# Kernel tuning notes

Hardware: AMD Instinct MI355X
Metric: run time of the kernel (lower is better)

Reference implementation:

```python
import jax, jax.numpy as jnp
import numpy as np

# ---- config (mirrors cfg in the torch module) ----
L_CIOU, L_CONF, L_CLS, L_ATTN = 2.0, 1.0, 1.0, 5.0
H_IN, W_IN, STRIDE, NUM_CLS = 1024, 1024, 4, 2
SIGMA = 1.5  # gaussian sigma for attention target
FOCAL_ALPHA, FOCAL_GAMMA = 0.25, 2.0
EPS = 1e-7


def setup_inputs() -> dict:
    key = jax.random.key(0)
    ks = jax.random.split(key, 6)
    B = 16
    fh, fw = H_IN // STRIDE, W_IN // STRIDE
    HW = fh * fw
    raw_grid = jax.random.normal(ks[0], (B, HW, 5 + NUM_CLS), dtype=jnp.float32)
    sal = jax.random.normal(ks[1], (B, 32, fh, fw), dtype=jnp.float32)
    N = 256
    bi = jax.random.randint(ks[2], (N,), 0, B).astype(jnp.float32)
    cxcy = jax.random.uniform(ks[3], (N, 2), minval=0.05, maxval=0.95)
    wh = jax.random.uniform(ks[4], (N, 2), minval=0.02, maxval=0.15)
    cls = jax.random.randint(ks[5], (N,), 0, NUM_CLS).astype(jnp.float32)
    targets = jnp.concatenate([bi[:, None], cxcy, wh, cls[:, None]], axis=1)
    return {"raw_grid": raw_grid, "sal": sal, "targets": targets}


def _ciou(p, t):
    """Complete IoU loss; p, t: (..., 4) cxcywh. Returns (...,)."""
    px1, py1 = p[..., 0] - p[..., 2] / 2, p[..., 1] - p[..., 3] / 2
    px2, py2 = p[..., 0] + p[..., 2] / 2, p[..., 1] + p[..., 3] / 2
    tx1, ty1 = t[..., 0] - t[..., 2] / 2, t[..., 1] - t[..., 3] / 2
    tx2, ty2 = t[..., 0] + t[..., 2] / 2, t[..., 1] + t[..., 3] / 2
    inter = (jnp.clip(jnp.minimum(px2, tx2) - jnp.maximum(px1, tx1), 0, None) *
             jnp.clip(jnp.minimum(py2, ty2) - jnp.maximum(py1, ty1), 0, None))
    union = p[..., 2] * p[..., 3] + t[..., 2] * t[..., 3] - inter
    iou = inter / (union + EPS)
    c2 = ((jnp.maximum(px2, tx2) - jnp.minimum(px1, tx1)) ** 2 +
          (jnp.maximum(py2, ty2) - jnp.minimum(py1, ty1)) ** 2 + EPS)
    d2 = (p[..., 0] - t[..., 0]) ** 2 + (p[..., 1] - t[..., 1]) ** 2
    v = (4.0 / (jnp.pi ** 2)) * (jnp.arctan(t[..., 2] / (t[..., 3] + EPS)) -
                                 jnp.arctan(p[..., 2] / (p[..., 3] + EPS))) ** 2
    alpha = jax.lax.stop_gradient(v / (1 - iou + v + EPS))
    return 1 - iou + d2 / c2 + alpha * v


def _decode_boxes(raw, fh, fw):
    """raw: (B, HW, 5+C) -> decoded boxes (B, HW, 4) and conf prob (B, HW)."""
    gy, gx = jnp.meshgrid(jnp.arange(fh, dtype=jnp.float32),
                          jnp.arange(fw, dtype=jnp.float32), indexing='ij')
    gx, gy = gx.reshape(-1), gy.reshape(-1)  # (HW,)
    cx = (jax.nn.sigmoid(raw[..., 0]) + gx) / fw
    cy = (jax.nn.sigmoid(raw[..., 1]) + gy) / fh
    w = jnp.exp(jnp.clip(raw[..., 2], -4, 4)) / fw
    h = jnp.exp(jnp.clip(raw[..., 3], -4, 4)) / fh
    conf = jax.nn.sigmoid(raw[..., 4])
    return jnp.stack([cx, cy, w, h], axis=-1), conf


def _assign(targets, B, fh, fw):
    """Vectorized FCOS-style assignment (replaces the per-target python loop).
    Each target emits 10 candidate writes: 3x3 neighborhood (conditioned on the
    cell centre lying inside the GT box) plus the unconditional centre cell.
    Last-write-wins semantics of the torch loop are reproduced with a
    scatter-max over a unique write priority."""
    N = targets.shape[0]
    HW = fh * fw
    bi = targets[:, 0].astype(jnp.int32)
    cx, cy, w, h = targets[:, 1], targets[:, 2], targets[:, 3], targets[:, 4]
    cls = targets[:, 5].astype(jnp.int32)
    gi = (cx * fw).astype(jnp.int32)
    gj = (cy * fh).astype(jnp.int32)
    dx = jnp.array([-1, -1, -1, 0, 0, 0, 1, 1, 1], jnp.int32)  # torch loop order
    dy = jnp.array([-1, 0, 1, -1, 0, 1, -1, 0, 1], jnp.int32)
    nx, ny = gi[:, None] + dx, gj[:, None] + dy               # (N, 9)
    inb = (nx >= 0) & (nx < fw) & (ny >= 0) & (ny < fh)
    ccx = (nx.astype(jnp.float32) + 0.5) / fw
    ccy = (ny.astype(jnp.float32) + 0.5) / fh
    inside = ((jnp.abs(ccx - cx[:, None]) <= w[:, None] / 2) &
              (jnp.abs(ccy - cy[:, None]) <= h[:, None] / 2))
    v9 = inb & inside
    c9 = ny * fw + nx
    cc = (jnp.minimum(gj, fh - 1) * fw + jnp.minimum(gi, fw - 1))[:, None]
    cells = jnp.concatenate([c9, cc], axis=1)                  # (N, 10)
    valid = jnp.concatenate([v9, jnp.ones((N, 1), bool)], axis=1)
    prio = (jnp.arange(N, dtype=jnp.int32)[:, None] * 10 +
            jnp.arange(10, dtype=jnp.int32)[None, :])          # unique per write
    PAD = B * HW
    flat = jnp.where(valid, bi[:, None] * HW + cells, PAD).reshape(-1)
    prio = jnp.where(valid, prio, -1).reshape(-1)
    win = jnp.full(PAD + 1, -1, jnp.int32).at[flat].max(prio)
    is_win = (prio >= 0) & (prio == win[flat])
    flat_w = jnp.where(is_win, flat, PAD)  # losers/invalid -> padding slot
    boxes = jnp.broadcast_to(targets[:, None, 1:5], (N, 10, 4)).reshape(-1, 4)
    tgt_box = jnp.zeros((PAD + 1, 4), jnp.float32).at[flat_w].set(boxes)[:PAD]
    clsb = jnp.broadcast_to(cls[:, None], (N, 10)).reshape(-1)
    tgt_cls = jnp.zeros(PAD + 1, jnp.int32).at[flat_w].set(clsb)[:PAD]
    obj = (win[:PAD] >= 0).astype(jnp.float32)
    return obj.reshape(B, HW), tgt_box.reshape(B, HW, 4), tgt_cls.reshape(B, HW)


def _attn_loss(sal, targets):
    """Batched Gaussian build + scatter-max (replaces per-target host loop)."""
    B, C, H, W = sal.shape
    gy, gx = jnp.meshgrid(jnp.arange(H, dtype=jnp.float32),
                          jnp.arange(W, dtype=jnp.float32), indexing='ij')
    bi = targets[:, 0].astype(jnp.int32)
    tx = targets[:, 1] * W
    ty = targets[:, 2] * H
    d2 = ((gx[None] - tx[:, None, None]) ** 2 +
          (gy[None] - ty[:, None, None]) ** 2)                 # (N, H, W)
    g = jnp.exp(-d2 / (2.0 * SIGMA ** 2))
    mask = jnp.zeros((B, H, W), jnp.float32).at[bi].max(g)     # scatter-max
    sal_mean = sal.mean(axis=1)                                # (B, H, W)
    return jnp.mean((sal_mean - mask) ** 2)


def reference(raw_grid, sal, targets):
    B, HW, _ = raw_grid.shape
    fh, fw = H_IN // STRIDE, W_IN // STRIDE
    loss_attn = _attn_loss(sal, targets)  # single saliency map (len==1 mean)

    pred_box, conf = _decode_boxes(raw_grid, fh, fw)
    obj, tgt_box, tgt_cls = _assign(targets, B, fh, fw)

    num_pos = jnp.sum(obj)
    norm = jnp.maximum(num_pos, 1.0)

    # focal BCE on confidence (all cells); stable via logits
    z = raw_grid[..., 4]
    bce = obj * jax.nn.softplus(-z) + (1 - obj) * jax.nn.softplus(z)
    pt = jnp.where(obj > 0, conf, 1 - conf)
    a_t = jnp.where(obj > 0, FOCAL_ALPHA, 1 - FOCAL_ALPHA)
    loss_conf = jnp.sum(a_t * (1 - pt) ** FOCAL_GAMMA * bce) / norm

    # CIoU over positive cells only (masked mean)
    loss_ciou = jnp.sum(_ciou(pred_box, tgt_box) * obj) / norm

    # cross-entropy over positive cells only
    logp = jax.nn.log_softmax(raw_grid[..., 5:], axis=-1)
    nll = -jnp.take_along_axis(logp, tgt_cls[..., None], axis=-1)[..., 0]
    loss_cls = jnp.sum(nll * obj) / norm

    return (L_CIOU * loss_ciou + L_CONF * loss_conf +
            L_CLS * loss_cls + L_ATTN * loss_attn)
```

## Files before the change

kernel.cpp:

```cpp
#include <hip/hip_runtime.h>
#include <math.h>

#define FH 256
#define FW 256
#define HW (FH * FW)
#define BATCH 16
#define NTGT 256
#define NCH 32
#define EPS_ 1e-7f

__device__ __forceinline__ float sigmoidf_(float x) {
    return 1.0f / (1.0f + expf(-x));
}
__device__ __forceinline__ float softplusf_(float x) {
    return fmaxf(x, 0.0f) + log1pf(expf(-fabsf(x)));
}

__global__ __launch_bounds__(256) void init_kernel(float* __restrict__ mask,
                                                   int* __restrict__ win) {
    int i = blockIdx.x * 256 + threadIdx.x;
    if (i < BATCH * HW) {
        mask[i] = 0.0f;
        win[i] = -1;
    }
}

__global__ __launch_bounds__(256) void scatter_kernel(const float* __restrict__ targets,
                                                      float* __restrict__ mask,
                                                      int* __restrict__ win) {
    int n = blockIdx.x;
    float bif = targets[n * 6 + 0];
    float cx  = targets[n * 6 + 1];
    float cy  = targets[n * 6 + 2];
    float w   = targets[n * 6 + 3];
    float h   = targets[n * 6 + 4];
    int bi = (int)bif;

    if (threadIdx.x == 0) {
        int gi = (int)(cx * (float)FW);
        int gj = (int)(cy * (float)FH);
#pragma unroll
        for (int k = 0; k < 9; ++k) {
            int dxv = k / 3 - 1;
            int dyv = k % 3 - 1;
            int nx = gi + dxv, ny = gj + dyv;
            bool inb = (nx >= 0) && (nx < FW) && (ny >= 0) && (ny < FH);
            float ccx = ((float)nx + 0.5f) / (float)FW;
            float ccy = ((float)ny + 0.5f) / (float)FH;
            bool inside = (fabsf(ccx - cx) <= w * 0.5f) && (fabsf(ccy - cy) <= h * 0.5f);
            if (inb && inside) {
                atomicMax(&win[bi * HW + ny * FW + nx], n * 10 + k);
            }
        }
        int cell = min(gj, FH - 1) * FW + min(gi, FW - 1);
        atomicMax(&win[bi * HW + cell], n * 10 + 9);
    }

    float tx = cx * (float)FW;
    float ty = cy * (float)FH;
    int itx = (int)tx, ity = (int)ty;
    int x0 = max(0, itx - 12), x1 = min(FW - 1, itx + 12);
    int y0 = max(0, ity - 12), y1 = min(FH - 1, ity + 12);
    int nxw = x1 - x0 + 1;
    int tot = nxw * (y1 - y0 + 1);
    unsigned int* mrow = (unsigned int*)(mask + bi * HW);
    for (int i = threadIdx.x; i < tot; i += blockDim.x) {
        int xx = x0 + i % nxw;
        int yy = y0 + i / nxw;
        float ddx = (float)xx - tx;
        float ddy = (float)yy - ty;
        float g = expf(-(ddx * ddx + ddy * ddy) / 4.5f);
        atomicMax(&mrow[yy * FW + xx], __float_as_uint(g));
    }
}

__global__ __launch_bounds__(256) void main_kernel(const float* __restrict__ raw,
                                                   const float* __restrict__ sal,
                                                   const float* __restrict__ targets,
                                                   const float* __restrict__ mask,
                                                   const int* __restrict__ win,
                                                   float* __restrict__ partials) {
    int p = blockIdx.x * 256 + threadIdx.x;
    int b = p >> 16;
    int hw = p & (HW - 1);

    const float* sp = sal + (size_t)b * NCH * HW + hw;
    float ssum = 0.0f;
#pragma unroll
    for (int c = 0; c < NCH; ++c) ssum += sp[(size_t)c * HW];
    float smean = ssum * (1.0f / 32.0f);
    float dm = smean - mask[p];
    float attn_t = dm * dm;

    const float* r = raw + (size_t)p * 7;
    float r0 = r[0], r1 = r[1], r2 = r[2], r3 = r[3];
    float z = r[4], l0 = r[5], l1 = r[6];

    int x = hw & (FW - 1);
    int y = hw >> 8;
    float pcx = (sigmoidf_(r0) + (float)x) / (float)FW;
    float pcy = (sigmoidf_(r1) + (float)y) / (float)FH;
    float pw = expf(fminf(fmaxf(r2, -4.0f), 4.0f)) / (float)FW;
    float ph = expf(fminf(fmaxf(r3, -4.0f), 4.0f)) / (float)FH;
    float conf = sigmoidf_(z);

    int wv = win[p];
    float conf_t, ciou_t = 0.0f, cls_t = 0.0f, posf;
    if (wv >= 0) {
        posf = 1.0f;
        float omc = 1.0f - conf;
        conf_t = 0.25f * omc * omc * softplusf_(-z);

        int t = wv / 10;
        float tcx = targets[t * 6 + 1], tcy = targets[t * 6 + 2];
        float tw = targets[t * 6 + 3], th = targets[t * 6 + 4];
        int cls = (int)targets[t * 6 + 5];

        float px1 = pcx - pw * 0.5f, py1 = pcy - ph * 0.5f;
        float px2 = pcx + pw * 0.5f, py2 = pcy + ph * 0.5f;
        float tx1 = tcx - tw * 0.5f, ty1 = tcy - th * 0.5f;
        float tx2 = tcx + tw * 0.5f, ty2 = tcy + th * 0.5f;
        float iw = fmaxf(fminf(px2, tx2) - fmaxf(px1, tx1), 0.0f);
        float ih = fmaxf(fminf(py2, ty2) - fmaxf(py1, ty1), 0.0f);
        float inter = iw * ih;
        float uni = pw * ph + tw * th - inter;
        float iou = inter / (uni + EPS_);
        float cw = fmaxf(px2, tx2) - fminf(px1, tx1);
        float chh = fmaxf(py2, ty2) - fminf(py1, ty1);
        float c2 = cw * cw + chh * chh + EPS_;
        float dcx = pcx - tcx, dcy = pcy - tcy;
        float d2 = dcx * dcx + dcy * dcy;
        float dv = atanf(tw / (th + EPS_)) - atanf(pw / (ph + EPS_));
        float v = (4.0f / (float)(M_PI * M_PI)) * dv * dv;
        float alpha = v / (1.0f - iou + v + EPS_);
        ciou_t = 1.0f - iou + d2 / c2 + alpha * v;

        float m_ = fmaxf(l0, l1);
        float lse = m_ + logf(expf(l0 - m_) + expf(l1 - m_));
        cls_t = lse - ((cls == 0) ? l0 : l1);
    } else {
        posf = 0.0f;
        conf_t = 0.75f * conf * conf * softplusf_(z);
    }

    float vals[5] = {attn_t, conf_t, ciou_t, cls_t, posf};
#pragma unroll
    for (int j = 0; j < 5; ++j) {
        float v = vals[j];
#pragma unroll
        for (int o = 32; o > 0; o >>= 1) v += __shfl_down(v, o, 64);
        vals[j] = v;
    }
    __shared__ float red[4][5];
    int lane = threadIdx.x & 63;
    int wid = threadIdx.x >> 6;
    if (lane == 0) {
#pragma unroll
        for (int j = 0; j < 5; ++j) red[wid][j] = vals[j];
    }
    __syncthreads();
    if (threadIdx.x == 0) {
#pragma unroll
        for (int j = 0; j < 5; ++j) {
            partials[blockIdx.x * 5 + j] = red[0][j] + red[1][j] + red[2][j] + red[3][j];
        }
    }
}

__global__ __launch_bounds__(256) void finalize_kernel(const float* __restrict__ partials,
                                                       int nblk, float* __restrict__ out) {
    __shared__ double red[256][5];
    double acc[5] = {0, 0, 0, 0, 0};
    for (int i = threadIdx.x; i < nblk; i += 256) {
#pragma unroll
        for (int j = 0; j < 5; ++j) acc[j] += (double)partials[i * 5 + j];
    }
#pragma unroll
    for (int j = 0; j < 5; ++j) red[threadIdx.x][j] = acc[j];
    __syncthreads();
    for (int s = 128; s > 0; s >>= 1) {
        if (threadIdx.x < s) {
#pragma unroll
            for (int j = 0; j < 5; ++j) red[threadIdx.x][j] += red[threadIdx.x + s][j];
        }
        __syncthreads();
    }
    if (threadIdx.x == 0) {
        double attn = red[0][0];
        double conf = red[0][1];
        double ciou = red[0][2];
        double cls = red[0][3];
        double npos = red[0][4];
        double norm = fmax(npos, 1.0);
        double loss = 2.0 * ciou / norm + 1.0 * conf / norm + 1.0 * cls / norm +
                      5.0 * (attn / (double)(BATCH * HW));
        out[0] = (float)loss;
    }
}

extern "C" void kernel_launch(void* const* d_in, const int* in_sizes, int n_in,
                              void* d_out, int out_size, void* d_ws, size_t ws_size,
                              hipStream_t stream) {
    const float* raw = (const float*)d_in[0];
    const float* sal = (const float*)d_in[1];
    const float* targets = (const float*)d_in[2];
    float* out = (float*)d_out;

    char* ws = (char*)d_ws;
    float* mask = (float*)ws;
    int* win = (int*)(ws + (size_t)BATCH * HW * sizeof(float));
    float* partials = (float*)(ws + (size_t)BATCH * HW * 8);

    const int NBLK = (BATCH * HW) / 256;

    init_kernel<<<NBLK, 256, 0, stream>>>(mask, win);
    scatter_kernel<<<NTGT, 256, 0, stream>>>(targets, mask, win);
    main_kernel<<<NBLK, 256, 0, stream>>>(raw, sal, targets, mask, win, partials);
    finalize_kernel<<<1, 256, 0, stream>>>(partials, NBLK, out);
}
```

Before: 222.8 us.

## Vectorize main kernel to four cells per thread and use atomic reduction

Each thread in the main kernel now handles four consecutive cells and reads saliency, mask, win and raw data with float4/int4 loads, so there are fewer, wider memory transactions and a quarter as many blocks. The per-block partials array and the 256-thread double-precision finalize reduction are replaced by float atomicAdd into a five-element accumulator and a one-thread finalize. The custom init kernel is replaced by hipMemsetAsync calls, one of which also zeroes the accumulator. The float atomics make the sum order nondeterministic and give up the double-precision final reduction.

```diff
diff --git a/kernel.cpp b/kernel.cpp
--- a/kernel.cpp
+++ b/kernel.cpp
@@ -16,25 +16,15 @@
     return fmaxf(x, 0.0f) + log1pf(expf(-fabsf(x)));
 }
 
-__global__ __launch_bounds__(256) void init_kernel(float* __restrict__ mask,
-                                                   int* __restrict__ win) {
-    int i = blockIdx.x * 256 + threadIdx.x;
-    if (i < BATCH * HW) {
-        mask[i] = 0.0f;
-        win[i] = -1;
-    }
-}
-
 __global__ __launch_bounds__(256) void scatter_kernel(const float* __restrict__ targets,
                                                       float* __restrict__ mask,
                                                       int* __restrict__ win) {
     int n = blockIdx.x;
-    float bif = targets[n * 6 + 0];
     float cx  = targets[n * 6 + 1];
     float cy  = targets[n * 6 + 2];
     float w   = targets[n * 6 + 3];
     float h   = targets[n * 6 + 4];
-    int bi = (int)bif;
+    int bi = (int)targets[n * 6 + 0];
 
     if (threadIdx.x == 0) {
         int gi = (int)(cx * (float)FW);
@@ -79,123 +69,118 @@
                                                    const float* __restrict__ targets,
                                                    const float* __restrict__ mask,
                                                    const int* __restrict__ win,
-                                                   float* __restrict__ partials) {
-    int p = blockIdx.x * 256 + threadIdx.x;
-    int b = p >> 16;
-    int hw = p & (HW - 1);
-
-    const float* sp = sal + (size_t)b * NCH * HW + hw;
-    float ssum = 0.0f;
-#pragma unroll
-    for (int c = 0; c < NCH; ++c) ssum += sp[(size_t)c * HW];
-    float smean = ssum * (1.0f / 32.0f);
-    float dm = smean - mask[p];
-    float attn_t = dm * dm;
-
-    const float* r = raw + (size_t)p * 7;
-    float r0 = r[0], r1 = r[1], r2 = r[2], r3 = r[3];
-    float z = r[4], l0 = r[5], l1 = r[6];
-
-    int x = hw & (FW - 1);
+                                                   float* __restrict__ acc) {
+    int q = blockIdx.x * 256 + threadIdx.x;
+    int base = q << 2;
+    int b = base >> 16;
+    int hw = base & (HW - 1);
+
+    const float4* sp = (const float4*)(sal + (size_t)b * NCH * HW + hw);
+    float4 s = make_float4(0.f, 0.f, 0.f, 0.f);
+#pragma unroll
+    for (int c = 0; c < NCH; ++c) {
+        float4 v = sp[(size_t)c * (HW / 4)];
+        s.x += v.x; s.y += v.y; s.z += v.z; s.w += v.w;
+    }
+    float4 mk = *(const float4*)(mask + base);
+    float sm[4]  = {s.x, s.y, s.z, s.w};
+    float mkv[4] = {mk.x, mk.y, mk.z, mk.w};
+
+    float4 rr[7];
+    const float4* rp = (const float4*)(raw + (size_t)base * 7);
+#pragma unroll
+    for (int i = 0; i < 7; ++i) rr[i] = rp[i];
+    const float* rf = (const float*)rr;
+
+    int4 wv4 = *(const int4*)(win + base);
+    int wvs[4] = {wv4.x, wv4.y, wv4.z, wv4.w};
+
+    float attn_s = 0.f, conf_s = 0.f, ciou_s = 0.f, cls_s = 0.f, pos_s = 0.f;
+    int x0i = hw & (FW - 1);
     int y = hw >> 8;
-    float pcx = (sigmoidf_(r0) + (float)x) / (float)FW;
-    float pcy = (sigmoidf_(r1) + (float)y) / (float)FH;
-    float pw = expf(fminf(fmaxf(r2, -4.0f), 4.0f)) / (float)FW;
-    float ph = expf(fminf(fmaxf(r3, -4.0f), 4.0f)) / (float)FH;
-    float conf = sigmoidf_(z);
-
-    int wv = win[p];
-    float conf_t, ciou_t = 0.0f, cls_t = 0.0f, posf;
-    if (wv >= 0) {
-        posf = 1.0f;
-        float omc = 1.0f - conf;
-        conf_t = 0.25f * omc * omc * softplusf_(-z);
-
-        int t = wv / 10;
-        float tcx = targets[t * 6 + 1], tcy = targets[t * 6 + 2];
-        float tw = targets[t * 6 + 3], th = targets[t * 6 + 4];
-        int cls = (int)targets[t * 6 + 5];
-
-        float px1 = pcx - pw * 0.5f, py1 = pcy - ph * 0.5f;
-        float px2 = pcx + pw * 0.5f, py2 = pcy + ph * 0.5f;
-        float tx1 = tcx - tw * 0.5f, ty1 = tcy - th * 0.5f;
-        float tx2 = tcx + tw * 0.5f, ty2 = tcy + th * 0.5f;
-        float iw = fmaxf(fminf(px2, tx2) - fmaxf(px1, tx1), 0.0f);
-        float ih = fmaxf(fminf(py2, ty2) - fmaxf(py1, ty1), 0.0f);
-        float inter = iw * ih;
-        float uni = pw * ph + tw * th - inter;
-        float iou = inter / (uni + EPS_);
-        float cw = fmaxf(px2, tx2) - fminf(px1, tx1);
-        float chh = fmaxf(py2, ty2) - fminf(py1, ty1);
-        float c2 = cw * cw + chh * chh + EPS_;
-        float dcx = pcx - tcx, dcy = pcy - tcy;
-        float d2 = dcx * dcx + dcy * dcy;
-        float dv = atanf(tw / (th + EPS_)) - atanf(pw / (ph + EPS_));
-        float v = (4.0f / (float)(M_PI * M_PI)) * dv * dv;
-        float alpha = v / (1.0f - iou + v + EPS_);
-        ciou_t = 1.0f - iou + d2 / c2 + alpha * v;
-
-        float m_ = fmaxf(l0, l1);
-        float lse = m_ + logf(expf(l0 - m_) + expf(l1 - m_));
-        cls_t = lse - ((cls == 0) ? l0 : l1);
-    } else {
-        posf = 0.0f;
-        conf_t = 0.75f * conf * conf * softplusf_(z);
-    }
-
-    float vals[5] = {attn_t, conf_t, ciou_t, cls_t, posf};
-#pragma unroll
-    for (int j = 0; j < 5; ++j) {
-        float v = vals[j];
+    float fy = (float)y;
+
+#pragma unroll
+    for (int j = 0; j < 4; ++j) {
+        float dmm = sm[j] * (1.0f / 32.0f) - mkv[j];
+        attn_s += dmm * dmm;
+
+        const float* r = rf + j * 7;
+        float r0 = r[0], r1 = r[1], r2 = r[2], r3 = r[3];
+        float z = r[4], l0 = r[5], l1 = r[6];
+
+        float pcx = (sigmoidf_(r0) + (float)(x0i + j)) * (1.0f / (float)FW);
+        float pcy = (sigmoidf_(r1) + fy) * (1.0f / (float)FH);
+        float pw = expf(fminf(fmaxf(r2, -4.0f), 4.0f)) * (1.0f / (float)FW);
+        float ph = expf(fminf(fmaxf(r3, -4.0f), 4.0f)) * (1.0f / (float)FH);
+        float conf = sigmoidf_(z);
+
+        int wv = wvs[j];
+        if (wv >= 0) {
+            pos_s += 1.0f;
+            float omc = 1.0f - conf;
+            conf_s += 0.25f * omc * omc * softplusf_(-z);
+
+            int t = wv / 10;
+            float tcx = targets[t * 6 + 1], tcy = targets[t * 6 + 2];
+            float tw = targets[t * 6 + 3], th = targets[t * 6 + 4];
+            int cls = (int)targets[t * 6 + 5];
+
+            float px1 = pcx - pw * 0.5f, py1 = pcy - ph * 0.5f;
+            float px2 = pcx + pw * 0.5f, py2 = pcy + ph * 0.5f;
+            float tx1 = tcx - tw * 0.5f, ty1 = tcy - th * 0.5f;
+            float tx2 = tcx + tw * 0.5f, ty2 = tcy + th * 0.5f;
+            float iw = fmaxf(fminf(px2, tx2) - fmaxf(px1, tx1), 0.0f);
+            float ih = fmaxf(fminf(py2, ty2) - fmaxf(py1, ty1), 0.0f);
+            float inter = iw * ih;
+            float uni = pw * ph + tw * th - inter;
+            float iou = inter / (uni + EPS_);
+            float cw = fmaxf(px2, tx2) - fminf(px1, tx1);
+            float chh = fmaxf(py2, ty2) - fminf(py1, ty1);
+            float c2 = cw * cw + chh * chh + EPS_;
+            float dcx = pcx - tcx, dcy = pcy - tcy;
+            float d2 = dcx * dcx + dcy * dcy;
+            float dv = atanf(tw / (th + EPS_)) - atanf(pw / (ph + EPS_));
+            float v = (4.0f / (float)(M_PI * M_PI)) * dv * dv;
+            float alpha = v / (1.0f - iou + v + EPS_);
+            ciou_s += 1.0f - iou + d2 / c2 + alpha * v;
+
+            float m_ = fmaxf(l0, l1);
+            float lse = m_ + logf(expf(l0 - m_) + expf(l1 - m_));
+            cls_s += lse - ((cls == 0) ? l0 : l1);
+        } else {
+            conf_s += 0.75f * conf * conf * softplusf_(z);
+        }
+    }
+
+    float vals[5] = {attn_s, conf_s, ciou_s, cls_s, pos_s};
+#pragma unroll
+    for (int jj = 0; jj < 5; ++jj) {
+        float v = vals[jj];
 #pragma unroll
         for (int o = 32; o > 0; o >>= 1) v += __shfl_down(v, o, 64);
-        vals[j] = v;
+        vals[jj] = v;
     }
     __shared__ float red[4][5];
     int lane = threadIdx.x & 63;
     int wid = threadIdx.x >> 6;
     if (lane == 0) {
 #pragma unroll
-        for (int j = 0; j < 5; ++j) red[wid][j] = vals[j];
+        for (int jj = 0; jj < 5; ++jj) red[wid][jj] = vals[jj];
     }
     __syncthreads();
-    if (threadIdx.x == 0) {
-#pragma unroll
-        for (int j = 0; j < 5; ++j) {
-            partials[blockIdx.x * 5 + j] = red[0][j] + red[1][j] + red[2][j] + red[3][j];
-        }
-    }
-}
-
-__global__ __launch_bounds__(256) void finalize_kernel(const float* __restrict__ partials,
-                                                       int nblk, float* __restrict__ out) {
-    __shared__ double red[256][5];
-    double acc[5] = {0, 0, 0, 0, 0};
-    for (int i = threadIdx.x; i < nblk; i += 256) {
-#pragma unroll
-        for (int j = 0; j < 5; ++j) acc[j] += (double)partials[i * 5 + j];
-    }
-#pragma unroll
-    for (int j = 0; j < 5; ++j) red[threadIdx.x][j] = acc[j];
-    __syncthreads();
-    for (int s = 128; s > 0; s >>= 1) {
-        if (threadIdx.x < s) {
-#pragma unroll
-            for (int j = 0; j < 5; ++j) red[threadIdx.x][j] += red[threadIdx.x + s][j];
-        }
-        __syncthreads();
-    }
-    if (threadIdx.x == 0) {
-        double attn = red[0][0];
-        double conf = red[0][1];
-        double ciou = red[0][2];
-        double cls = red[0][3];
-        double npos = red[0][4];
-        double norm = fmax(npos, 1.0);
-        double loss = 2.0 * ciou / norm + 1.0 * conf / norm + 1.0 * cls / norm +
-                      5.0 * (attn / (double)(BATCH * HW));
-        out[0] = (float)loss;
-    }
+    if (threadIdx.x < 5) {
+        float v = red[0][threadIdx.x] + red[1][threadIdx.x] +
+                  red[2][threadIdx.x] + red[3][threadIdx.x];
+        atomicAdd(&acc[threadIdx.x], v);
+    }
+}
+
+__global__ void finalize_kernel(const float* __restrict__ acc, float* __restrict__ out) {
+    float attn = acc[0], conf = acc[1], ciou = acc[2], cls = acc[3], npos = acc[4];
+    float norm = fmaxf(npos, 1.0f);
+    out[0] = (2.0f * ciou + conf + cls) / norm +
+             5.0f * (attn * (1.0f / (float)(BATCH * HW)));
 }
 
 extern "C" void kernel_launch(void* const* d_in, const int* in_sizes, int n_in,
@@ -208,13 +193,13 @@
 
     char* ws = (char*)d_ws;
     float* mask = (float*)ws;
-    int* win = (int*)(ws + (size_t)BATCH * HW * sizeof(float));
-    float* partials = (float*)(ws + (size_t)BATCH * HW * 8);
-
-    const int NBLK = (BATCH * HW) / 256;
-
-    init_kernel<<<NBLK, 256, 0, stream>>>(mask, win);
+    float* acc = (float*)(ws + (size_t)BATCH * HW * sizeof(float));
+    int* win = (int*)(ws + (size_t)BATCH * HW * sizeof(float) + 256);
+
+    hipMemsetAsync(mask, 0, (size_t)BATCH * HW * sizeof(float) + 256, stream);
+    hipMemsetAsync(win, 0xFF, (size_t)BATCH * HW * sizeof(int), stream);
+
     scatter_kernel<<<NTGT, 256, 0, stream>>>(targets, mask, win);
-    main_kernel<<<NBLK, 256, 0, stream>>>(raw, sal, targets, mask, win, partials);
-    finalize_kernel<<<1, 256, 0, stream>>>(partials, NBLK, out);
-}
+    main_kernel<<<(BATCH * HW / 4) / 256, 256, 0, stream>>>(raw, sal, targets, mask, win, acc);
+    finalize_kernel<<<1, 1, 0, stream>>>(acc, out);
+}
```

Measured after the change: 227.0 us. No clear change (+1.9%).
